# Kernel tuning notes

Measured on AMD Instinct MI355X. Metric: run time of the kernel, lower is better.

## Reference

```python
import jax, jax.numpy as jnp
import numpy as np

CD_COEFF = 1.0  # init_kwargs cd_coeff

def _chamfer(p1, p2):
    # p1: (B, N, 3), p2: (B, M, 3)
    # pairwise squared distances (B, N, M)
    d2 = jnp.sum((p1[:, :, None, :] - p2[:, None, :, :]) ** 2, axis=-1)
    d = jnp.sqrt(d2)  # L2 norm as in torch.norm(dist, 2, dim=3)
    min_nm = jnp.min(d, axis=2)  # (B, N): for each pred point, nearest target
    min_mn = jnp.min(d, axis=1)  # (B, M): for each target point, nearest pred
    # batch-normalized symmetric chamfer distance
    return jnp.mean(jnp.mean(min_nm, axis=1) + jnp.mean(min_mn, axis=1))

def setup_inputs() -> dict:
    key = jax.random.key(0)
    k1, k2 = jax.random.split(key)
    x_diff_pred = jax.random.normal(k1, (8, 4096, 3), dtype=jnp.float32)
    x_diff_target = jax.random.normal(k2, (8, 4096, 3), dtype=jnp.float32)
    return {"x_diff_pred": x_diff_pred, "x_diff_target": x_diff_target}

def reference(x_diff_pred, x_diff_target):
    cd = _chamfer(x_diff_pred, x_diff_target)
    loss = CD_COEFF * cd
    return loss
```

## Files before the change

### kernel.cpp

```cpp
#include <hip/hip_runtime.h>


typedef _Float16 f16x4 __attribute__((ext_vector_type(4)));
typedef float    f32x16 __attribute__((ext_vector_type(16)));

#define BATCH 8
#define NPTS 4096
#define THREADS 512
#define HALF_PTS 2048
#define HALF_TILES 64
#define NSLOT 65536
#define K1_BLOCKS 256
#define RBLKS 256

__device__ __forceinline__ float min3f(float a, float b, float c) {
    return fminf(fminf(a, b), c);
}

__global__ __launch_bounds__(THREADS, 4) void cd_mfma(
        const float* __restrict__ pred,
        const float* __restrict__ targ,
        float* __restrict__ P) {
    __shared__ unsigned long long sdb[HALF_PTS * 2];
    const int bx   = blockIdx.x;
    const int tid  = threadIdx.x;
    const int dirb = bx >> 4;
    const int qg   = (bx >> 1) & 7;
    const int h    = bx & 1;
    const int wave = tid >> 6;
    const int lane = tid & 63;
    const int dir  = dirb >> 3;
    const int b    = dirb & 7;
    const float* Qraw = (dir ? targ : pred) + (size_t)b * NPTS * 3;
    const float* Draw = (dir ? pred : targ) + (size_t)b * NPTS * 3;

    for (int i = tid; i < HALF_PTS; i += THREADS) {
        const float* p = Draw + (size_t)(h * HALF_PTS + i) * 3;
        _Float16 hx = (_Float16)p[0], hy = (_Float16)p[1], hz = (_Float16)p[2];
        float xf = (float)hx, yf = (float)hy, zf = (float)hz;
        float w  = fmaf(xf, xf, fmaf(yf, yf, zf * zf));
        _Float16 hhi = (_Float16)w;
        _Float16 hlo = (_Float16)(w - (float)hhi);
        f16x4 lo4 = {hx, hy, hz, hhi};
        f16x4 hi4 = {hlo, (_Float16)0.f, (_Float16)0.f, (_Float16)0.f};
        const int t = i >> 5, r = i & 31;
        sdb[t * 64 + r]      = __builtin_bit_cast(unsigned long long, lo4);
        sdb[t * 64 + 32 + r] = __builtin_bit_cast(unsigned long long, hi4);
    }

    const int q0 = qg * 512 + wave * 64 + (lane & 31);
    const int q1 = q0 + 32;
    float nq0, nq1;
    auto mkB = [&](int q, float& nq) -> f16x4 {
        const float* qp = Qraw + (size_t)q * 3;
        _Float16 qx = (_Float16)qp[0], qy = (_Float16)qp[1], qz = (_Float16)qp[2];
        float xr = (float)qx, yr = (float)qy, zr = (float)qz;
        nq = fmaf(xr, xr, fmaf(yr, yr, zr * zr));
        _Float16 mx = (_Float16)(-2.f * xr), my = (_Float16)(-2.f * yr),
                 mz = (_Float16)(-2.f * zr), one = (_Float16)1.f,
                 zz = (_Float16)0.f;
        return (lane < 32) ? (f16x4){mx, my, mz, one}
                           : (f16x4){one, zz, zz, zz};
    };
    f16x4 B0 = mkB(q0, nq0);
    f16x4 B1 = mkB(q1, nq1);

    __syncthreads();

    const f32x16 Z = {};
    const float inf = __uint_as_float(0x7F800000u);
    float m0 = inf, m1 = inf;
    auto fold = [&](const f32x16& a, float& m) {
        float s0 = min3f(a[0],  a[1],  a[2]);
        float s1 = min3f(a[3],  a[4],  a[5]);
        float s2 = min3f(a[6],  a[7],  a[8]);
        float s3 = min3f(a[9],  a[10], a[11]);
        float s4 = min3f(a[12], a[13], a[14]);
        float t0 = min3f(s0, s1, s2);
        float t1 = min3f(s3, s4, a[15]);
        m = min3f(m, t0, t1);
    };

    int idx = lane;
    auto rdA = [&]() {
        f16x4 v = __builtin_bit_cast(f16x4, sdb[idx]);
        idx += 64;
        return v;
    };

    f16x4 A0 = rdA();
    f32x16 a00 = __builtin_amdgcn_mfma_f32_32x32x8f16(A0, B0, Z, 0, 0, 0);
    f32x16 a01 = __builtin_amdgcn_mfma_f32_32x32x8f16(A0, B1, Z, 0, 0, 0);
    f16x4 A1 = rdA();
    f32x16 a10 = __builtin_amdgcn_mfma_f32_32x32x8f16(A1, B0, Z, 0, 0, 0);
    f32x16 a11 = __builtin_amdgcn_mfma_f32_32x32x8f16(A1, B1, Z, 0, 0, 0);
    #pragma unroll 4
    for (int j = 2; j < HALF_TILES; j += 2) {
        f16x4 An = rdA();
        fold(a00, m0); fold(a01, m1);
        a00 = __builtin_amdgcn_mfma_f32_32x32x8f16(An, B0, Z, 0, 0, 0);
        a01 = __builtin_amdgcn_mfma_f32_32x32x8f16(An, B1, Z, 0, 0, 0);
        f16x4 Am = rdA();
        fold(a10, m0); fold(a11, m1);
        a10 = __builtin_amdgcn_mfma_f32_32x32x8f16(Am, B0, Z, 0, 0, 0);
        a11 = __builtin_amdgcn_mfma_f32_32x32x8f16(Am, B1, Z, 0, 0, 0);
    }
    fold(a00, m0); fold(a01, m1);
    fold(a10, m0); fold(a11, m1);

    m0 = fminf(m0, __shfl_xor(m0, 32, 64));
    m1 = fminf(m1, __shfl_xor(m1, 32, 64));
    if (lane < 32) {
        float* Ph = P + (size_t)h * NSLOT + (size_t)dirb * NPTS;
        Ph[q0] = m0 + nq0;
        Ph[q1] = m1 + nq1;
    }
}

__global__ __launch_bounds__(256) void cd_red(
        const float* __restrict__ P, float* __restrict__ Bsum) {
    const int tid  = threadIdx.x;
    const int slot = blockIdx.x * 256 + tid;
    float v = fminf(P[slot], P[NSLOT + slot]);
    float d = sqrtf(fmaxf(v, 0.f));
    #pragma unroll
    for (int off = 32; off > 0; off >>= 1) d += __shfl_down(d, off);
    __shared__ float wsum[4];
    if ((tid & 63) == 0) wsum[tid >> 6] = d;
    __syncthreads();
    if (tid == 0)
        Bsum[blockIdx.x] = (wsum[0] + wsum[1]) + (wsum[2] + wsum[3]);
}

__global__ __launch_bounds__(256) void cd_final(
        const float* __restrict__ Bsum, float* __restrict__ out) {
    const int tid = threadIdx.x;
    float s = Bsum[tid];
    __shared__ float red[256];
    red[tid] = s;
    __syncthreads();
    for (int off = 128; off > 0; off >>= 1) {
        if (tid < off) red[tid] += red[tid + off];
        __syncthreads();
    }
    if (tid == 0) out[0] = red[0] * (1.0f / (float)(BATCH * NPTS));
}

extern "C" void kernel_launch(void* const* d_in, const int* in_sizes, int n_in,
                              void* d_out, int out_size, void* d_ws, size_t ws_size,
                              hipStream_t stream) {
    const float* pred = (const float*)d_in[0];
    const float* targ = (const float*)d_in[1];
    float* P    = (float*)d_ws;
    float* Bsum = (float*)((char*)d_ws + 2 * NSLOT * 4);
    float* out  = (float*)d_out;

    cd_mfma<<<K1_BLOCKS, THREADS, 0, stream>>>(pred, targ, P);
    cd_red<<<RBLKS, 256, 0, stream>>>(P, Bsum);
    cd_final<<<1, 256, 0, stream>>>(Bsum, out);
}
```

Baseline: 16.27 us.

## Fuse half-split min reduction into MFMA kernel, drop intermediate reduce kernel

Each block now loads the full 4096-point database into LDS and splits it across two wave groups instead of splitting it across two blocks. Each block handles 256 queries, combines the two partial minima through shared memory, then takes the sqrt and sums per block in-kernel. This removes the global partial-min buffer and the separate cd_red launch. The costs are a doubled LDS footprint (64KB), which may lower occupancy, twice the staging work per block, and an extra block barrier.

```diff
diff --git a/kernel.cpp b/kernel.cpp
--- a/kernel.cpp
+++ b/kernel.cpp
@@ -7,11 +7,8 @@
 #define BATCH 8
 #define NPTS 4096
 #define THREADS 512
-#define HALF_PTS 2048
 #define HALF_TILES 64
-#define NSLOT 65536
 #define K1_BLOCKS 256
-#define RBLKS 256
 
 __device__ __forceinline__ float min3f(float a, float b, float c) {
     return fminf(fminf(a, b), c);
@@ -20,22 +17,25 @@
 __global__ __launch_bounds__(THREADS, 4) void cd_mfma(
         const float* __restrict__ pred,
         const float* __restrict__ targ,
-        float* __restrict__ P) {
-    __shared__ unsigned long long sdb[HALF_PTS * 2];
+        float* __restrict__ Bsum) {
+    __shared__ unsigned long long sdb[NPTS * 2];
+    __shared__ float wpA[4][64], wpB[4][64];
+    __shared__ float wred[4];
     const int bx   = blockIdx.x;
     const int tid  = threadIdx.x;
     const int dirb = bx >> 4;
-    const int qg   = (bx >> 1) & 7;
-    const int h    = bx & 1;
+    const int qg   = bx & 15;
     const int wave = tid >> 6;
     const int lane = tid & 63;
+    const int wsel = wave & 3;
+    const int hsel = wave >> 2;
     const int dir  = dirb >> 3;
     const int b    = dirb & 7;
     const float* Qraw = (dir ? targ : pred) + (size_t)b * NPTS * 3;
     const float* Draw = (dir ? pred : targ) + (size_t)b * NPTS * 3;
 
-    for (int i = tid; i < HALF_PTS; i += THREADS) {
-        const float* p = Draw + (size_t)(h * HALF_PTS + i) * 3;
+    for (int i = tid; i < NPTS; i += THREADS) {
+        const float* p = Draw + (size_t)i * 3;
         _Float16 hx = (_Float16)p[0], hy = (_Float16)p[1], hz = (_Float16)p[2];
         float xf = (float)hx, yf = (float)hy, zf = (float)hz;
         float w  = fmaf(xf, xf, fmaf(yf, yf, zf * zf));
@@ -48,7 +48,7 @@
         sdb[t * 64 + 32 + r] = __builtin_bit_cast(unsigned long long, hi4);
     }
 
-    const int q0 = qg * 512 + wave * 64 + (lane & 31);
+    const int q0 = qg * 256 + wsel * 64 + (lane & 31);
     const int q1 = q0 + 32;
     float nq0, nq1;
     auto mkB = [&](int q, float& nq) -> f16x4 {
@@ -81,7 +81,7 @@
         m = min3f(m, t0, t1);
     };
 
-    int idx = lane;
+    int idx = hsel * (HALF_TILES * 64) + lane;
     auto rdA = [&]() {
         f16x4 v = __builtin_bit_cast(f16x4, sdb[idx]);
         idx += 64;
@@ -111,25 +111,30 @@
     m0 = fminf(m0, __shfl_xor(m0, 32, 64));
     m1 = fminf(m1, __shfl_xor(m1, 32, 64));
     if (lane < 32) {
-        float* Ph = P + (size_t)h * NSLOT + (size_t)dirb * NPTS;
-        Ph[q0] = m0 + nq0;
-        Ph[q1] = m1 + nq1;
+        float (*wp)[64] = hsel ? wpB : wpA;
+        wp[wsel][lane]      = m0;
+        wp[wsel][32 + lane] = m1;
     }
-}
-
-__global__ __launch_bounds__(256) void cd_red(
-        const float* __restrict__ P, float* __restrict__ Bsum) {
-    const int tid  = threadIdx.x;
-    const int slot = blockIdx.x * 256 + tid;
-    float v = fminf(P[slot], P[NSLOT + slot]);
-    float d = sqrtf(fmaxf(v, 0.f));
-    #pragma unroll
-    for (int off = 32; off > 0; off >>= 1) d += __shfl_down(d, off);
-    __shared__ float wsum[4];
-    if ((tid & 63) == 0) wsum[tid >> 6] = d;
+    __syncthreads();
+    if (wave < 4) {
+        const int l = lane & 31;
+        float d = 0.f;
+        if (lane < 32) {
+            float mm0 = fminf(wpA[wave][l],      wpB[wave][l]);
+            float mm1 = fminf(wpA[wave][32 + l], wpB[wave][32 + l]);
+            d = sqrtf(fmaxf(mm0 + nq0, 0.f)) + sqrtf(fmaxf(mm1 + nq1, 0.f));
+        }
+        d += __shfl_xor(d, 32, 64);
+        d += __shfl_xor(d, 16, 64);
+        d += __shfl_xor(d,  8, 64);
+        d += __shfl_xor(d,  4, 64);
+        d += __shfl_xor(d,  2, 64);
+        d += __shfl_xor(d,  1, 64);
+        if (lane == 0) wred[wave] = d;
+    }
     __syncthreads();
     if (tid == 0)
-        Bsum[blockIdx.x] = (wsum[0] + wsum[1]) + (wsum[2] + wsum[3]);
+        Bsum[bx] = (wred[0] + wred[1]) + (wred[2] + wred[3]);
 }
 
 __global__ __launch_bounds__(256) void cd_final(
@@ -151,11 +156,9 @@
                               hipStream_t stream) {
     const float* pred = (const float*)d_in[0];
     const float* targ = (const float*)d_in[1];
-    float* P    = (float*)d_ws;
-    float* Bsum = (float*)((char*)d_ws + 2 * NSLOT * 4);
+    float* Bsum = (float*)d_ws;
     float* out  = (float*)d_out;
 
-    cd_mfma<<<K1_BLOCKS, THREADS, 0, stream>>>(pred, targ, P);
-    cd_red<<<RBLKS, 256, 0, stream>>>(P, Bsum);
+    cd_mfma<<<K1_BLOCKS, THREADS, 0, stream>>>(pred, targ, Bsum);
     cd_final<<<1, 256, 0, stream>>>(Bsum, out);
 }
```

Measured after the change: 16.17 us. No clear change (-0.6%).
